# Kernel tuning notes

Measured on AMD Instinct MI355X. Metric: run time of the kernel, lower is better.

## Reference

```python
import jax, jax.numpy as jnp
import numpy as np

B, T, D, UNITS = 64, 512, 256, 1024
SCALE = 0.05  # small init so gate pre-activations stay in a sane range


def setup_inputs() -> dict:
    key = jax.random.key(0)
    k1, k2, k3 = jax.random.split(key, 3)
    x = jax.random.normal(k1, (B, T, D), dtype=jnp.float32)
    W = jax.random.normal(k2, (D, 4 * UNITS), dtype=jnp.float32) * SCALE
    U = jax.random.normal(k3, (UNITS, 4 * UNITS), dtype=jnp.float32) * SCALE
    b = jnp.zeros((4 * UNITS,), dtype=jnp.float32)
    return {"x": x, "W": W, "U": U, "b": b}


def _lstm(x, W, U, b):
    # Keras LSTM, gate order i|f|g(candidate)|o, recurrent_activation=sigmoid,
    # activation=tanh. recurrent_dropout is inactive at inference (training=None).
    units = U.shape[0]
    batch = x.shape[0]
    h0 = jnp.zeros((batch, units), x.dtype)
    c0 = jnp.zeros((batch, units), x.dtype)
    # Precompute input projections for all timesteps in one big GEMM.
    xz = jnp.einsum('btd,dg->btg', x, W) + b  # [B, T, 4*units]
    xz_t = jnp.swapaxes(xz, 0, 1)             # [T, B, 4*units]

    def step(carry, xz_step):
        h, c = carry
        z = xz_step + h @ U                    # [B, 4*units]
        i, f, g, o = jnp.split(z, 4, axis=-1)
        i = jax.nn.sigmoid(i)
        f = jax.nn.sigmoid(f)
        g = jnp.tanh(g)
        o = jax.nn.sigmoid(o)
        c_new = f * c + i * g
        h_new = o * jnp.tanh(c_new)
        return (h_new, c_new), h_new

    (h_last, c_last), hs = jax.lax.scan(step, (h0, c0), xz_t)
    seq = jnp.swapaxes(hs, 0, 1)               # [B, T, units]
    return seq, h_last, c_last


def reference(x, W, U, b):
    # Encoder.call: returns (output, hidden_state, cell_state);
    # return_sequences=True -> output is the full hidden-state sequence.
    return _lstm(x, W, U, b)
```

## Files before the change

kernel.cpp:

```cpp
#include <hip/hip_runtime.h>
#include <hip/hip_bf16.h>
#include <cstdint>
#include <cstddef>


#define SEQ_N  33554432

typedef __attribute__((ext_vector_type(8))) short short8;
typedef __attribute__((ext_vector_type(4))) float floatx4;

#define BMFMA __builtin_amdgcn_mfma_f32_16x16x32_bf16

static __device__ __forceinline__ short f2bf(float f) {
  __hip_bfloat16 h = __float2bfloat16(f);
  return *reinterpret_cast<short*>(&h);
}
static __device__ __forceinline__ float sigm(float x) { return 1.f / (1.f + __expf(-x)); }
static __device__ __forceinline__ float tanh_fast(float x) {
  float xc = fminf(fmaxf(x, -15.f), 15.f);
  float e  = __expf(2.f * xc);
  return (e - 1.f) / (e + 1.f);
}

__global__ void pack_weights(const float* __restrict__ W, const float* __restrict__ U,
                             short* __restrict__ upack) {
  int idx  = blockIdx.x * 256 + threadIdx.x;
  int lane = idx & 63;
  int frag = idx >> 6;
  int kk   = frag % 40;
  int ct   = (frag / 40) & 7;
  int ug   = frag / 320;
  int quad = lane >> 4, n = lane & 15;
  int col  = (n >> 2) * 1024 + ug * 32 + ct * 4 + (n & 3);
  int k0   = kk * 32 + quad * 8;
  short8 v;
#pragma unroll
  for (int j = 0; j < 8; ++j) {
    int k = k0 + j;
    float f = (k < 1024) ? U[(size_t)k * 4096 + col] : W[(size_t)(k - 1024) * 4096 + col];
    v[j] = f2bf(f);
  }
  *reinterpret_cast<short8*>(upack + (size_t)idx * 8) = v;
}

__global__ void convert_x(const float* __restrict__ x, short* __restrict__ xbf) {
  int idx = blockIdx.x * 256 + threadIdx.x;
  const float* xp = x + (size_t)idx * 8;
  short8 v;
#pragma unroll
  for (int j = 0; j < 8; ++j) v[j] = f2bf(xp[j]);
  *reinterpret_cast<short8*>(xbf + (size_t)idx * 8) = v;
}

__global__ void init_state(unsigned int* __restrict__ base) {
  int idx = blockIdx.x * 256 + threadIdx.x;
  if (idx < 65808)
    __hip_atomic_store(&base[idx], 0u, __ATOMIC_RELAXED, __HIP_MEMORY_SCOPE_AGENT);
}

__global__ __launch_bounds__(256, 1) void lstm_persist(
    const short* __restrict__ xbf,
    const short* __restrict__ upack,
    const float* __restrict__ bias,
    char* __restrict__ hx,
    int* __restrict__ arrive,
    const short* __restrict__ zb,
    float* __restrict__ out)
{
  __shared__ short hlds[16384];
  __shared__ float zlds[8][8][17];

  const int m    = blockIdx.x >> 5;
  const int slot = blockIdx.x & 31;
  const int ub   = slot * 32;

  const int tid  = threadIdx.x;
  const int wave = tid >> 6;
  const int lane = tid & 63;
  const int quad = lane >> 4;
  const int l15  = lane & 15;
  const int te   = 2 * wave, to = 2 * wave + 1;

  const int erow = tid >> 5;
  const int us   = tid & 31;
  const int ui   = us & 3, ct_e = us >> 2;
  const int unit = ub + us;
  const float bi = bias[unit],        bfv = bias[1024 + unit];
  const float bg = bias[2048 + unit], bo  = bias[3072 + unit];
  float cst = 0.f;

  const short* wbase = upack + (size_t)slot * (8 * 40 * 64 * 8);
  short8 wUe[32], wUo[32];
#pragma unroll
  for (int ks = 0; ks < 32; ++ks) {
    wUe[ks] = *reinterpret_cast<const short8*>(wbase + (((size_t)te * 40 + ks) * 64 + lane) * 8);
    wUo[ks] = *reinterpret_cast<const short8*>(wbase + (((size_t)to * 40 + ks) * 64 + lane) * 8);
  }
  {
    int r = 8 + (tid >> 5), seg = tid & 31;
    short8 z = {0, 0, 0, 0, 0, 0, 0, 0};
    const int sw = (r & 7) << 4;
#pragma unroll
    for (int j = 0; j < 4; ++j) {
      int b = seg * 16 + j * 512;
      *reinterpret_cast<short8*>((char*)hlds + r * 2048 + (b ^ sw)) = z;
    }
  }
  __syncthreads();

  floatx4 xe0, xe1, xo0, xo1;
  auto xw = [&](int t) {
    floatx4 z4 = {0.f, 0.f, 0.f, 0.f};
    floatx4 e0 = z4, e1 = z4, o0 = z4, o1 = z4;
    const short* xr = (l15 < 8)
        ? xbf + (((size_t)(8 * m + l15) * 512 + t) * 256 + quad * 8)
        : zb + quad * 8;
    const int xstep = (l15 < 8) ? 32 : 0;
    const short* wbe = wbase + (((size_t)te * 40 + 32) * 64 + lane) * 8;
    const short* wbo = wbase + (((size_t)to * 40 + 32) * 64 + lane) * 8;
#pragma unroll
    for (int ks = 0; ks < 8; ++ks) {
      short8 A  = *reinterpret_cast<const short8*>(xr); xr += xstep;
      short8 Be = *reinterpret_cast<const short8*>(wbe + ks * 512);
      short8 Bo = *reinterpret_cast<const short8*>(wbo + ks * 512);
      if (ks & 1) { e1 = BMFMA(A, Be, e1, 0, 0, 0); o1 = BMFMA(A, Bo, o1, 0, 0, 0); }
      else        { e0 = BMFMA(A, Be, e0, 0, 0, 0); o0 = BMFMA(A, Bo, o0, 0, 0, 0); }
    }
    xe0 = e0; xe1 = e1; xo0 = o0; xo1 = o1;
  };
  xw(0);

  const int stage_r = tid >> 5, stage_seg = tid & 31;
  int* flagp = arrive + m * 32;

  for (int t = 0; t < 512; ++t) {
    if (t > 0 && wave == 0) {
      for (;;) {
        int v = (lane < 32)
                  ? __hip_atomic_load(flagp + lane, __ATOMIC_RELAXED,
                                      __HIP_MEMORY_SCOPE_AGENT)
                  : t;
        if (__all(v >= t)) break;
      }
    }
    __syncthreads();
    {
      const char* src = hx + ((size_t)(m * 2 + (t & 1)) << 14)
                      + stage_r * 2048 + stage_seg * 16;
      short8 v0, v1, v2, v3;
      asm volatile("global_load_dwordx4 %0, %4, off sc0 sc1\n\t"
                   "global_load_dwordx4 %1, %4, off offset:512 sc0 sc1\n\t"
                   "global_load_dwordx4 %2, %4, off offset:1024 sc0 sc1\n\t"
                   "global_load_dwordx4 %3, %4, off offset:1536 sc0 sc1\n\t"
                   "s_waitcnt vmcnt(0)"
                   : "=&v"(v0), "=&v"(v1), "=&v"(v2), "=&v"(v3)
                   : "v"(src) : "memory");
      char* dbase = (char*)hlds + stage_r * 2048;
      const int sw = (stage_r & 7) << 4;
      const int b0 = stage_seg * 16;
      *reinterpret_cast<short8*>(dbase + ((b0       ) ^ sw)) = v0;
      *reinterpret_cast<short8*>(dbase + ((b0 +  512) ^ sw)) = v1;
      *reinterpret_cast<short8*>(dbase + ((b0 + 1024) ^ sw)) = v2;
      *reinterpret_cast<short8*>(dbase + ((b0 + 1536) ^ sw)) = v3;
    }
    __syncthreads();
    floatx4 aE0 = xe0, aE1 = xe1, aO0 = xo0, aO1 = xo1;
    {
      const char* hb = (const char*)hlds + l15 * 2048;
      const int rx = (l15 & 7) << 4;
#pragma unroll
      for (int ks = 0; ks < 32; ++ks) {
        short8 A = *reinterpret_cast<const short8*>(hb + ((ks * 64 + quad * 16) ^ rx));
        if (ks & 1) { aE1 = BMFMA(A, wUe[ks], aE1, 0, 0, 0); aO1 = BMFMA(A, wUo[ks], aO1, 0, 0, 0); }
        else        { aE0 = BMFMA(A, wUe[ks], aE0, 0, 0, 0); aO0 = BMFMA(A, wUo[ks], aO0, 0, 0, 0); }
      }
    }
    floatx4 aE = aE0 + aE1, aO = aO0 + aO1;
    if (quad < 2) {
#pragma unroll
      for (int i = 0; i < 4; ++i) {
        int row = quad * 4 + i;
        zlds[row][te][l15] = aE[i];
        zlds[row][to][l15] = aO[i];
      }
    }
    __syncthreads();
    float zi = zlds[erow][ct_e][0 + ui] + bi;
    float zf = zlds[erow][ct_e][4 + ui] + bfv;
    float zg = zlds[erow][ct_e][8 + ui] + bg;
    float zo = zlds[erow][ct_e][12 + ui] + bo;
    float ig = sigm(zi), fg = sigm(zf), gg = tanh_fast(zg), og = sigm(zo);
    cst = fg * cst + ig * gg;
    float hn = og * tanh_fast(cst);

    if (t < 511) {
      float hn1 = __shfl_xor(hn, 1);
      unsigned int p01 = (unsigned int)(unsigned short)f2bf(hn) |
                         ((unsigned int)(unsigned short)f2bf(hn1) << 16);
      unsigned int pot = __shfl_xor(p01, 2);
      if (ui == 0) {
        unsigned long long v = (unsigned long long)p01 |
                               ((unsigned long long)pot << 32);
        unsigned long long* dst = (unsigned long long*)
            (hx + ((size_t)(m * 2 + ((t + 1) & 1)) << 14)
                + erow * 2048 + (size_t)(ub + (us & ~3)) * 2);
        __hip_atomic_store(dst, v, __ATOMIC_RELAXED, __HIP_MEMORY_SCOPE_AGENT);
      }
      asm volatile("s_waitcnt vmcnt(0)" ::: "memory");
      __syncthreads();
      if (tid == 0)
        __hip_atomic_store(flagp + slot, t + 1, __ATOMIC_RELAXED,
                           __HIP_MEMORY_SCOPE_AGENT);
      out[((size_t)(8 * m + erow) * 512 + t) * 1024 + unit] = hn;
      xw(t + 1);
    } else {
      size_t gr = 8 * m + erow;
      out[(gr * 512 + 511) * 1024 + unit] = hn;
      out[(size_t)SEQ_N + gr * 1024 + unit] = hn;
      out[(size_t)SEQ_N + 65536 + gr * 1024 + unit] = cst;
    }
  }
}

extern "C" void kernel_launch(void* const* d_in, const int* in_sizes, int n_in,
                              void* d_out, int out_size, void* d_ws, size_t ws_size,
                              hipStream_t stream) {
  const float* x    = (const float*)d_in[0];
  const float* W    = (const float*)d_in[1];
  const float* U    = (const float*)d_in[2];
  const float* bias = (const float*)d_in[3];
  float* out = (float*)d_out;
  char* ws = (char*)d_ws;

  short* upack = (short*)ws;
  short* xbf   = (short*)(ws + 10485760);
  char*  hx    = ws + 27262976;
  int*   arrive= (int*)(ws + 27525120);
  short* zb    = (short*)(ws + 27526144);
  (void)in_sizes; (void)n_in; (void)out_size; (void)ws_size;

  init_state<<<258, 256, 0, stream>>>((unsigned int*)(ws + 27262976));
  pack_weights<<<2560, 256, 0, stream>>>(W, U, upack);
  convert_x<<<4096, 256, 0, stream>>>(x, xbf);
  lstm_persist<<<256, 256, 0, stream>>>(xbf, upack, bias, hx, arrive, zb, out);
}
```

Baseline: 2.470 ms.

## Replace arrival flags with tagged h-state words polled directly by consumers

Removes the separate per-slot arrival flag array and the store-wait-barrier-flag sequence. Each hidden-state 8-byte store now carries a timestep tag in its upper word, and consumers poll the h buffer itself until every tag matches, then pack the data into LDS in a new swizzled layout. Loads for the next step are issued speculatively right after the store, which overlaps them with the input projection. The trade-off is double the h buffer traffic for tags and repeated full-buffer reloads while spinning.

Result: slower. 2.838 ms (+14.9%).

```diff
diff --git a/kernel.cpp b/kernel.cpp
--- a/kernel.cpp
+++ b/kernel.cpp
@@ -8,6 +8,8 @@
 
 typedef __attribute__((ext_vector_type(8))) short short8;
 typedef __attribute__((ext_vector_type(4))) float floatx4;
+typedef __attribute__((ext_vector_type(4))) int   intx4;
+typedef __attribute__((ext_vector_type(2))) int   intx2;
 
 #define BMFMA __builtin_amdgcn_mfma_f32_16x16x32_bf16
 
@@ -52,18 +54,38 @@
   *reinterpret_cast<short8*>(xbf + (size_t)idx * 8) = v;
 }
 
-__global__ void init_state(unsigned int* __restrict__ base) {
+__global__ void init_state(unsigned int* __restrict__ hx32) {
   int idx = blockIdx.x * 256 + threadIdx.x;
-  if (idx < 65808)
-    __hip_atomic_store(&base[idx], 0u, __ATOMIC_RELAXED, __HIP_MEMORY_SCOPE_AGENT);
-}
+  if (idx < 131072) {
+    int within = idx & 16383;
+    unsigned int v = 0u;
+    if ((within >> 13) == 1 && (idx & 1)) v = 0xFFFFFFFFu;
+    __hip_atomic_store(&hx32[idx], v, __ATOMIC_RELAXED, __HIP_MEMORY_SCOPE_AGENT);
+  } else if (idx < 131088) {
+    __hip_atomic_store(&hx32[idx], 0u, __ATOMIC_RELAXED, __HIP_MEMORY_SCOPE_AGENT);
+  }
+}
+
+#define ISSUE8(SB)                                                          \
+  asm volatile(                                                             \
+    "global_load_dwordx4 %0, %8, %16 sc0 sc1\n\t"                           \
+    "global_load_dwordx4 %1, %9, %16 sc0 sc1\n\t"                           \
+    "global_load_dwordx4 %2, %10, %16 sc0 sc1\n\t"                          \
+    "global_load_dwordx4 %3, %11, %16 sc0 sc1\n\t"                          \
+    "global_load_dwordx4 %4, %12, %16 sc0 sc1\n\t"                          \
+    "global_load_dwordx4 %5, %13, %16 sc0 sc1\n\t"                          \
+    "global_load_dwordx4 %6, %14, %16 sc0 sc1\n\t"                          \
+    "global_load_dwordx4 %7, %15, %16 sc0 sc1"                              \
+    : "=&v"(L0), "=&v"(L1), "=&v"(L2), "=&v"(L3),                           \
+      "=&v"(L4), "=&v"(L5), "=&v"(L6), "=&v"(L7)                            \
+    : "v"(vo0), "v"(vo1), "v"(vo2), "v"(vo3),                               \
+      "v"(vo4), "v"(vo5), "v"(vo6), "v"(vo7), "s"(SB) : "memory")
 
 __global__ __launch_bounds__(256, 1) void lstm_persist(
     const short* __restrict__ xbf,
     const short* __restrict__ upack,
     const float* __restrict__ bias,
     char* __restrict__ hx,
-    int* __restrict__ arrive,
     const short* __restrict__ zb,
     float* __restrict__ out)
 {
@@ -97,14 +119,9 @@
     wUo[ks] = *reinterpret_cast<const short8*>(wbase + (((size_t)to * 40 + ks) * 64 + lane) * 8);
   }
   {
-    int r = 8 + (tid >> 5), seg = tid & 31;
     short8 z = {0, 0, 0, 0, 0, 0, 0, 0};
-    const int sw = (r & 7) << 4;
-#pragma unroll
-    for (int j = 0; j < 4; ++j) {
-      int b = seg * 16 + j * 512;
-      *reinterpret_cast<short8*>((char*)hlds + r * 2048 + (b ^ sw)) = z;
-    }
+    for (int i = tid; i < 2048; i += 256)
+      *reinterpret_cast<short8*>((char*)hlds + i * 16) = z;
   }
   __syncthreads();
 
@@ -130,50 +147,64 @@
   };
   xw(0);
 
-  const int stage_r = tid >> 5, stage_seg = tid & 31;
-  int* flagp = arrive + m * 32;
+  const unsigned long long sb0 = (unsigned long long)(hx + ((size_t)m << 16));
+  const unsigned long long sb1 = sb0 + 32768ull;
+  const unsigned int vo0 = tid * 16,          vo1 = tid * 16 + 4096;
+  const unsigned int vo2 = tid * 16 + 8192,   vo3 = tid * 16 + 12288;
+  const unsigned int vo4 = tid * 16 + 16384,  vo5 = tid * 16 + 20480;
+  const unsigned int vo6 = tid * 16 + 24576,  vo7 = tid * 16 + 28672;
+  char* db[8];
+#pragma unroll
+  for (int j = 0; j < 8; ++j) {
+    int g     = tid * 16 + j * 4096;
+    int seg   = g >> 7;
+    int srow  = seg >> 5, sslot = seg & 31;
+    int jj    = (g >> 4) & 7;
+    db[j] = (char*)hlds + sslot * 1024 + (jj >> 1) * 256
+          + ((srow ^ (sslot & 7)) << 4) + (jj & 1) * 8;
+  }
+  char* pb = hx + ((size_t)m << 16) + (size_t)(erow * 32 + slot) * 128 + (us >> 1) * 8;
+
+  intx4 L0, L1, L2, L3, L4, L5, L6, L7;
+  ISSUE8(sb0);
 
   for (int t = 0; t < 512; ++t) {
-    if (t > 0 && wave == 0) {
+    const unsigned long long sbt = (t & 1) ? sb1 : sb0;
+    {
+      const int T = t;
       for (;;) {
-        int v = (lane < 32)
-                  ? __hip_atomic_load(flagp + lane, __ATOMIC_RELAXED,
-                                      __HIP_MEMORY_SCOPE_AGENT)
-                  : t;
-        if (__all(v >= t)) break;
+        asm volatile("s_waitcnt vmcnt(0)" ::: "memory");
+        __builtin_amdgcn_sched_barrier(0);
+        int bad = (L0[1]^T)|(L0[3]^T)|(L1[1]^T)|(L1[3]^T)
+                | (L2[1]^T)|(L2[3]^T)|(L3[1]^T)|(L3[3]^T)
+                | (L4[1]^T)|(L4[3]^T)|(L5[1]^T)|(L5[3]^T)
+                | (L6[1]^T)|(L6[3]^T)|(L7[1]^T)|(L7[3]^T);
+        if (bad == 0) break;
+        ISSUE8(sbt);
       }
+      intx2 d0 = {L0[0], L0[2]}, d1 = {L1[0], L1[2]};
+      intx2 d2 = {L2[0], L2[2]}, d3 = {L3[0], L3[2]};
+      intx2 d4 = {L4[0], L4[2]}, d5 = {L5[0], L5[2]};
+      intx2 d6 = {L6[0], L6[2]}, d7 = {L7[0], L7[2]};
+      *reinterpret_cast<intx2*>(db[0]) = d0;
+      *reinterpret_cast<intx2*>(db[1]) = d1;
+      *reinterpret_cast<intx2*>(db[2]) = d2;
+      *reinterpret_cast<intx2*>(db[3]) = d3;
+      *reinterpret_cast<intx2*>(db[4]) = d4;
+      *reinterpret_cast<intx2*>(db[5]) = d5;
+      *reinterpret_cast<intx2*>(db[6]) = d6;
+      *reinterpret_cast<intx2*>(db[7]) = d7;
     }
     __syncthreads();
-    {
-      const char* src = hx + ((size_t)(m * 2 + (t & 1)) << 14)
-                      + stage_r * 2048 + stage_seg * 16;
-      short8 v0, v1, v2, v3;
-      asm volatile("global_load_dwordx4 %0, %4, off sc0 sc1\n\t"
-                   "global_load_dwordx4 %1, %4, off offset:512 sc0 sc1\n\t"
-                   "global_load_dwordx4 %2, %4, off offset:1024 sc0 sc1\n\t"
-                   "global_load_dwordx4 %3, %4, off offset:1536 sc0 sc1\n\t"
-                   "s_waitcnt vmcnt(0)"
-                   : "=&v"(v0), "=&v"(v1), "=&v"(v2), "=&v"(v3)
-                   : "v"(src) : "memory");
-      char* dbase = (char*)hlds + stage_r * 2048;
-      const int sw = (stage_r & 7) << 4;
-      const int b0 = stage_seg * 16;
-      *reinterpret_cast<short8*>(dbase + ((b0       ) ^ sw)) = v0;
-      *reinterpret_cast<short8*>(dbase + ((b0 +  512) ^ sw)) = v1;
-      *reinterpret_cast<short8*>(dbase + ((b0 + 1024) ^ sw)) = v2;
-      *reinterpret_cast<short8*>(dbase + ((b0 + 1536) ^ sw)) = v3;
-    }
-    __syncthreads();
+
     floatx4 aE0 = xe0, aE1 = xe1, aO0 = xo0, aO1 = xo1;
-    {
-      const char* hb = (const char*)hlds + l15 * 2048;
-      const int rx = (l15 & 7) << 4;
-#pragma unroll
-      for (int ks = 0; ks < 32; ++ks) {
-        short8 A = *reinterpret_cast<const short8*>(hb + ((ks * 64 + quad * 16) ^ rx));
-        if (ks & 1) { aE1 = BMFMA(A, wUe[ks], aE1, 0, 0, 0); aO1 = BMFMA(A, wUo[ks], aO1, 0, 0, 0); }
-        else        { aE0 = BMFMA(A, wUe[ks], aE0, 0, 0, 0); aO0 = BMFMA(A, wUo[ks], aO0, 0, 0, 0); }
-      }
+#pragma unroll
+    for (int ks = 0; ks < 32; ++ks) {
+      int rp = (l15 & 8) | ((l15 & 7) ^ (ks & 7));
+      short8 A = *reinterpret_cast<const short8*>(
+          (char*)hlds + ks * 1024 + quad * 256 + rp * 16);
+      if (ks & 1) { aE1 = BMFMA(A, wUe[ks], aE1, 0, 0, 0); aO1 = BMFMA(A, wUo[ks], aO1, 0, 0, 0); }
+      else        { aE0 = BMFMA(A, wUe[ks], aE0, 0, 0, 0); aO0 = BMFMA(A, wUo[ks], aO0, 0, 0, 0); }
     }
     floatx4 aE = aE0 + aE1, aO = aO0 + aO1;
     if (quad < 2) {
@@ -197,21 +228,14 @@
       float hn1 = __shfl_xor(hn, 1);
       unsigned int p01 = (unsigned int)(unsigned short)f2bf(hn) |
                          ((unsigned int)(unsigned short)f2bf(hn1) << 16);
-      unsigned int pot = __shfl_xor(p01, 2);
-      if (ui == 0) {
+      if ((us & 1) == 0) {
         unsigned long long v = (unsigned long long)p01 |
-                               ((unsigned long long)pot << 32);
-        unsigned long long* dst = (unsigned long long*)
-            (hx + ((size_t)(m * 2 + ((t + 1) & 1)) << 14)
-                + erow * 2048 + (size_t)(ub + (us & ~3)) * 2);
-        __hip_atomic_store(dst, v, __ATOMIC_RELAXED, __HIP_MEMORY_SCOPE_AGENT);
+                               ((unsigned long long)(unsigned int)(t + 1) << 32);
+        __hip_atomic_store((unsigned long long*)(pb + (((t + 1) & 1) << 15)), v,
+                           __ATOMIC_RELAXED, __HIP_MEMORY_SCOPE_AGENT);
       }
-      asm volatile("s_waitcnt vmcnt(0)" ::: "memory");
-      __syncthreads();
-      if (tid == 0)
-        __hip_atomic_store(flagp + slot, t + 1, __ATOMIC_RELAXED,
-                           __HIP_MEMORY_SCOPE_AGENT);
       out[((size_t)(8 * m + erow) * 512 + t) * 1024 + unit] = hn;
+      ISSUE8((t & 1) ? sb0 : sb1);
       xw(t + 1);
     } else {
       size_t gr = 8 * m + erow;
@@ -235,12 +259,11 @@
   short* upack = (short*)ws;
   short* xbf   = (short*)(ws + 10485760);
   char*  hx    = ws + 27262976;
-  int*   arrive= (int*)(ws + 27525120);
-  short* zb    = (short*)(ws + 27526144);
+  short* zb    = (short*)(ws + 27787264);
   (void)in_sizes; (void)n_in; (void)out_size; (void)ws_size;
 
-  init_state<<<258, 256, 0, stream>>>((unsigned int*)(ws + 27262976));
+  init_state<<<513, 256, 0, stream>>>((unsigned int*)hx);
   pack_weights<<<2560, 256, 0, stream>>>(W, U, upack);
   convert_x<<<4096, 256, 0, stream>>>(x, xbf);
-  lstm_persist<<<256, 256, 0, stream>>>(xbf, upack, bias, hx, arrive, zb, out);
-}
+  lstm_persist<<<256, 256, 0, stream>>>(xbf, upack, bias, hx, zb, out);
+}
```

## Map batch groups to XCDs and sync via XCD-local cache flags

Applied to the files above, without the earlier changes.

Each block reads its hardware XCC ID and claims a slot within that XCD through an atomic counter, so all 32 blocks sharing one batch group run on the same XCD. The per-step hidden-state exchange and arrival flags then use sc0-only (XCD-local L2) loads and stores instead of device-coherent sc0 sc1 accesses, which should cut cross-XCD coherence latency on the recurrent critical path. A slow device-scope path with a second set of flags is kept as a fallback after a spin timeout. The grid is enlarged to 384 blocks so every XCD has enough, and surplus blocks exit; this relies on block placement and co-residency assumptions.

Measured after the change: 2.457 ms. Within noise of the previous version (-0.6%).

```diff
diff --git a/kernel.cpp b/kernel.cpp
--- a/kernel.cpp
+++ b/kernel.cpp
@@ -54,7 +54,7 @@
 
 __global__ void init_state(unsigned int* __restrict__ base) {
   int idx = blockIdx.x * 256 + threadIdx.x;
-  if (idx < 65808)
+  if (idx < 66192)
     __hip_atomic_store(&base[idx], 0u, __ATOMIC_RELAXED, __HIP_MEMORY_SCOPE_AGENT);
 }
 
@@ -63,18 +63,32 @@
     const short* __restrict__ upack,
     const float* __restrict__ bias,
     char* __restrict__ hx,
-    int* __restrict__ arrive,
+    int* __restrict__ fastf,
+    int* __restrict__ slowf,
+    int* __restrict__ ctr,
     const short* __restrict__ zb,
     float* __restrict__ out)
 {
   __shared__ short hlds[16384];
   __shared__ float zlds[8][8][17];
-
-  const int m    = blockIdx.x >> 5;
-  const int slot = blockIdx.x & 31;
+  __shared__ int   slot_sh;
+  __shared__ int   use_slow_sh;
+
+  int xcd;
+  asm volatile("s_getreg_b32 %0, hwreg(HW_REG_XCC_ID)" : "=s"(xcd));
+  const int m   = xcd & 7;
+  const int tid = threadIdx.x;
+
+  if (tid == 0) {
+    slot_sh = __hip_atomic_fetch_add(&ctr[m * 16], 1,
+                                     __ATOMIC_RELAXED, __HIP_MEMORY_SCOPE_AGENT);
+    use_slow_sh = 0;
+  }
+  __syncthreads();
+  const int slot = slot_sh;
+  if (slot >= 32) return;
   const int ub   = slot * 32;
 
-  const int tid  = threadIdx.x;
   const int wave = tid >> 6;
   const int lane = tid & 63;
   const int quad = lane >> 4;
@@ -131,30 +145,60 @@
   xw(0);
 
   const int stage_r = tid >> 5, stage_seg = tid & 31;
-  int* flagp = arrive + m * 32;
+  int* ffp = fastf + m * 32 + (lane & 31);
+  int* sfp = slowf + m * 32 + (lane & 31);
+  int* ffs = fastf + m * 32 + slot;
+  int* sfs = slowf + m * 32 + slot;
 
   for (int t = 0; t < 512; ++t) {
-    if (t > 0 && wave == 0) {
-      for (;;) {
-        int v = (lane < 32)
-                  ? __hip_atomic_load(flagp + lane, __ATOMIC_RELAXED,
-                                      __HIP_MEMORY_SCOPE_AGENT)
-                  : t;
-        if (__all(v >= t)) break;
-      }
-    }
-    __syncthreads();
+    if (t > 0) {
+      if (wave == 0) {
+        int uslow = use_slow_sh;
+        if (!uslow) {
+          int cnt = 0;
+          for (;;) {
+            int v;
+            asm volatile("global_load_dword %0, %1, off sc0\n\t"
+                         "s_waitcnt vmcnt(0)"
+                         : "=v"(v) : "v"(ffp) : "memory");
+            if (__all(v >= t)) break;
+            if (++cnt > 8192) { uslow = 1; break; }
+          }
+          if (uslow && lane == 0) use_slow_sh = 1;
+        }
+        if (uslow) {
+          for (;;) {
+            int v;
+            asm volatile("global_load_dword %0, %1, off sc0 sc1\n\t"
+                         "s_waitcnt vmcnt(0)"
+                         : "=v"(v) : "v"(sfp) : "memory");
+            if (__all(v >= t)) break;
+          }
+        }
+      }
+      __syncthreads();
+    }
     {
       const char* src = hx + ((size_t)(m * 2 + (t & 1)) << 14)
                       + stage_r * 2048 + stage_seg * 16;
       short8 v0, v1, v2, v3;
-      asm volatile("global_load_dwordx4 %0, %4, off sc0 sc1\n\t"
-                   "global_load_dwordx4 %1, %4, off offset:512 sc0 sc1\n\t"
-                   "global_load_dwordx4 %2, %4, off offset:1024 sc0 sc1\n\t"
-                   "global_load_dwordx4 %3, %4, off offset:1536 sc0 sc1\n\t"
-                   "s_waitcnt vmcnt(0)"
-                   : "=&v"(v0), "=&v"(v1), "=&v"(v2), "=&v"(v3)
-                   : "v"(src) : "memory");
+      if (!use_slow_sh) {
+        asm volatile("global_load_dwordx4 %0, %4, off sc0\n\t"
+                     "global_load_dwordx4 %1, %4, off offset:512 sc0\n\t"
+                     "global_load_dwordx4 %2, %4, off offset:1024 sc0\n\t"
+                     "global_load_dwordx4 %3, %4, off offset:1536 sc0\n\t"
+                     "s_waitcnt vmcnt(0)"
+                     : "=&v"(v0), "=&v"(v1), "=&v"(v2), "=&v"(v3)
+                     : "v"(src) : "memory");
+      } else {
+        asm volatile("global_load_dwordx4 %0, %4, off sc0 sc1\n\t"
+                     "global_load_dwordx4 %1, %4, off offset:512 sc0 sc1\n\t"
+                     "global_load_dwordx4 %2, %4, off offset:1024 sc0 sc1\n\t"
+                     "global_load_dwordx4 %3, %4, off offset:1536 sc0 sc1\n\t"
+                     "s_waitcnt vmcnt(0)"
+                     : "=&v"(v0), "=&v"(v1), "=&v"(v2), "=&v"(v3)
+                     : "v"(src) : "memory");
+      }
       char* dbase = (char*)hlds + stage_r * 2048;
       const int sw = (stage_r & 7) << 4;
       const int b0 = stage_seg * 16;
@@ -201,18 +245,23 @@
       if (ui == 0) {
         unsigned long long v = (unsigned long long)p01 |
                                ((unsigned long long)pot << 32);
-        unsigned long long* dst = (unsigned long long*)
-            (hx + ((size_t)(m * 2 + ((t + 1) & 1)) << 14)
-                + erow * 2048 + (size_t)(ub + (us & ~3)) * 2);
-        __hip_atomic_store(dst, v, __ATOMIC_RELAXED, __HIP_MEMORY_SCOPE_AGENT);
-      }
+        char* dst = hx + ((size_t)(m * 2 + ((t + 1) & 1)) << 14)
+                  + erow * 2048 + (size_t)(ub + (us & ~3)) * 2;
+        asm volatile("global_store_dwordx2 %0, %1, off sc0\n\t"
+                     "global_store_dwordx2 %0, %1, off sc0 sc1"
+                     :: "v"(dst), "v"(v) : "memory");
+      }
+      asm volatile("s_waitcnt vmcnt(1)" ::: "memory");
+      __syncthreads();
+      int tv = t + 1;
+      if (tid == 0)
+        asm volatile("global_store_dword %0, %1, off sc0" :: "v"(ffs), "v"(tv) : "memory");
+      out[((size_t)(8 * m + erow) * 512 + t) * 1024 + unit] = hn;
+      xw(t + 1);
       asm volatile("s_waitcnt vmcnt(0)" ::: "memory");
       __syncthreads();
       if (tid == 0)
-        __hip_atomic_store(flagp + slot, t + 1, __ATOMIC_RELAXED,
-                           __HIP_MEMORY_SCOPE_AGENT);
-      out[((size_t)(8 * m + erow) * 512 + t) * 1024 + unit] = hn;
-      xw(t + 1);
+        asm volatile("global_store_dword %0, %1, off sc0 sc1" :: "v"(sfs), "v"(tv) : "memory");
     } else {
       size_t gr = 8 * m + erow;
       out[(gr * 512 + 511) * 1024 + unit] = hn;
@@ -235,12 +284,14 @@
   short* upack = (short*)ws;
   short* xbf   = (short*)(ws + 10485760);
   char*  hx    = ws + 27262976;
-  int*   arrive= (int*)(ws + 27525120);
-  short* zb    = (short*)(ws + 27526144);
+  int*   fastf = (int*)(ws + 27525120);
+  int*   slowf = (int*)(ws + 27526144);
+  int*   ctr   = (int*)(ws + 27527168);
+  short* zb    = (short*)(ws + 27527680);
   (void)in_sizes; (void)n_in; (void)out_size; (void)ws_size;
 
-  init_state<<<258, 256, 0, stream>>>((unsigned int*)(ws + 27262976));
+  init_state<<<259, 256, 0, stream>>>((unsigned int*)(ws + 27262976));
   pack_weights<<<2560, 256, 0, stream>>>(W, U, upack);
   convert_x<<<4096, 256, 0, stream>>>(x, xbf);
-  lstm_persist<<<256, 256, 0, stream>>>(xbf, upack, bias, hx, arrive, zb, out);
-}
+  lstm_persist<<<384, 256, 0, stream>>>(xbf, upack, bias, hx, fastf, slowf, ctr, zb, out);
+}
```
